# Optimization experiments

Measured on AMD Instinct MI355X. Metric: run time of the kernel, lower is better.

Reference implementation:

```python
import jax, jax.numpy as jnp
import numpy as np

RF = 13          # receptive field with defaults
N_LAYERS = 8     # blocks(4) * layers(2)
DIMS = 32
RC = 16          # residual/dilation channels
SC = 8           # skip channels
BN_EPS = 1e-5


def conv1x1(x, W, b=None):
    # x: (B,Cin,N,T), W: (Cout,Cin)
    y = jnp.einsum('oc,bcnt->bont', W, x)
    if b is not None:
        y = y + b[None, :, None, None]
    return y


def bn_eval(x, g, b):
    # eval-mode BatchNorm2d with running_mean=0, running_var=1
    return x * (g / jnp.sqrt(1.0 + BN_EPS))[None, :, None, None] + b[None, :, None, None]


def setup_inputs() -> dict:
    key = jax.random.key(0)
    ks = jax.random.split(key, 24)
    B, N, T, days = 16, 1024, 12, 288
    inp = {}
    inp['inputs'] = jax.random.normal(ks[0], (B, 2, N, T), dtype=jnp.float32)
    inp['ind'] = jax.random.randint(ks[1], (B,), 0, days)
    # start convs (1 -> RC)
    inp['start_w'] = jax.random.normal(ks[2], (RC, 1)) * 0.05
    inp['start_b'] = jax.random.normal(ks[3], (RC,)) * 0.05
    inp['starta_w'] = jax.random.normal(ks[4], (RC, 1)) * 0.05
    inp['starta_b'] = jax.random.normal(ks[5], (RC,)) * 0.05
    # dynamic-graph node embeddings (torch.randn init)
    inp['p1'] = jax.random.normal(ks[6], (days, DIMS))
    inp['p2'] = jax.random.normal(ks[7], (N, DIMS))
    inp['p3'] = jax.random.normal(ks[8], (N, DIMS))
    inp['pk'] = jax.random.normal(ks[9], (DIMS, DIMS, DIMS))
    # shared channel-attention fcs (bias=False)
    inp['fc1_w'] = jax.random.normal(ks[10], (RC, RC)) * 0.05
    inp['fc2_w'] = jax.random.normal(ks[11], (RC, RC)) * 0.05
    # per-layer skip convs (RC -> SC)
    inp['skip_w'] = jax.random.normal(ks[12], (N_LAYERS, SC, RC)) * 0.05
    inp['skip_b'] = jax.random.normal(ks[13], (N_LAYERS, SC)) * 0.05
    # per-layer gcn mlp ((order*support_len+1)*RC = 48 -> RC)
    inp['gconv_w'] = jax.random.normal(ks[14], (N_LAYERS, RC, 3 * RC)) * 0.05
    inp['gconv_b'] = jax.random.normal(ks[15], (N_LAYERS, RC)) * 0.05
    # batchnorm affine params
    inp['bn_g'] = jnp.ones((N_LAYERS, RC)) + jax.random.normal(ks[16], (N_LAYERS, RC)) * 0.01
    inp['bn_b'] = jax.random.normal(ks[17], (N_LAYERS, RC)) * 0.01
    inp['bna_g'] = jnp.ones((N_LAYERS, RC)) + jax.random.normal(ks[18], (N_LAYERS, RC)) * 0.01
    inp['bna_b'] = jax.random.normal(ks[19], (N_LAYERS, RC)) * 0.01
    # end convs: 832 -> 64 -> 12
    inp['end1_w'] = jax.random.normal(ks[20], (64, SC * RF * N_LAYERS)) * 0.02
    inp['end1_b'] = jax.random.normal(ks[21], (64,)) * 0.02
    inp['end2_w'] = jax.random.normal(ks[22], (12, 64)) * 0.02
    inp['end2_b'] = jax.random.normal(ks[23], (12,)) * 0.02
    return inp


def reference(inputs, ind, start_w, start_b, starta_w, starta_b, p1, p2, p3, pk,
              fc1_w, fc2_w, skip_w, skip_b, gconv_w, gconv_b,
              bn_g, bn_b, bna_g, bna_b, end1_w, end1_b, end2_w, end2_b):
    B, _, N, T = inputs.shape
    if T < RF:  # static python condition
        xo = jnp.pad(inputs, ((0, 0), (0, 0), (0, 0), (RF - T, 0)))
    else:
        xo = inputs
    x = conv1x1(xo[:, 0:1], start_w, start_b)      # (B,RC,N,RF)
    x_a = conv1x1(xo[:, 1:2], starta_w, starta_b)  # (B,RC,N,RF)

    # dgconstruct: dynamic adjacency (identical for every layer -> compute once)
    te = p1[ind]                                   # (B,DIMS)
    adp = jnp.einsum('ai,ijk->ajk', te, pk)        # (B,DIMS,DIMS)
    src = jnp.einsum('bj,ajk->abk', p2, adp)       # (B,N,DIMS)
    full = jnp.einsum('ck,abk->abc', p3, src)      # (B,N,N)
    temp = full[:, :, :DIMS]                       # (B,N,DIMS)
    x1 = jnp.einsum('bnd,bmd->bnm', src, temp)     # (B,N,N)
    A = jax.nn.relu(jnp.tanh(x1 - jnp.swapaxes(x1, 1, 2)))  # x2 = x1^T

    skips = []
    for i in range(N_LAYERS):
        residual = x
        # avg-pool / max-pool to same size are identity -> avg_out == max_out
        a_out = conv1x1(jax.nn.relu(conv1x1(residual, fc1_w)), fc2_w)
        x = jax.nn.sigmoid(a_out + a_out + x)
        residual_a = x_a
        s = conv1x1(x, skip_w[i], skip_b[i])        # (B,SC,N,RF)
        skips.append(jnp.transpose(s, (0, 1, 3, 2)).reshape(B, SC * RF, N, 1))
        # gcn with support_len=1, order=2 (dropout off in eval)
        h1 = jnp.einsum('bcvl,bwv->bcwl', x, A)
        h2 = jnp.einsum('bcvl,bwv->bcwl', h1, A)
        h = jnp.concatenate([x, h1, h2], axis=1)    # (B,3*RC,N,RF)
        x = conv1x1(h, gconv_w[i], gconv_b[i])
        x = x_a + x
        x_a = x_a + residual_a
        x = x + residual
        x = bn_eval(x, bn_g[i], bn_b[i])
        x_a = bn_eval(x_a, bna_g[i], bna_b[i])

    # torch prepends each new skip: last layer's skip goes first
    skip = jnp.concatenate(skips[::-1], axis=1)     # (B,832,N,1)
    out = jax.nn.relu(skip)
    out = jax.nn.relu(conv1x1(out, end1_w, end1_b))
    out = conv1x1(out, end2_w, end2_b)              # (B,12,N,1)
    return out
```

## Files before the change

### kernel.cpp

```cpp
#include <hip/hip_runtime.h>
#include <math.h>

#define NB 16
#define NCH 16
#define NL 13
#define NN 1024
#define NT 12
#define NLAY 8
#define MROWS 208
#define MPAD 256

typedef _Float16 f16;
typedef __attribute__((ext_vector_type(8))) _Float16 f16x8;
typedef __attribute__((ext_vector_type(16))) float f32x16;

#define OFF_TAB   0
#define OFF_SRC   1024
#define OFF_TEMP  (OFF_SRC  + (size_t)NB*NN*32)
#define OFF_AH    (OFF_TEMP + (size_t)NB*NN*32)
#define OFF_XH    (OFF_AH   + (size_t)NB*NN*NN/2)
#define OFF_XL    (OFF_XH   + (size_t)NB*MPAD*NN/2)
#define OFF_H1H   (OFF_XL   + (size_t)NB*MPAD*NN/2)
#define OFF_H1L   (OFF_H1H  + (size_t)NB*MPAD*NN/2)
#define OFF_H2    (OFF_H1L  + (size_t)NB*MPAD*NN/2)
#define OFF_X     (OFF_H2   + (size_t)NB*MPAD*NN)
#define OFF_SKIP  (OFF_X    + (size_t)NB*MROWS*NN)
#define WS_FLOATS (OFF_SKIP + (size_t)NB*832*NN)

__device__ __forceinline__ void gload16(const void* g, void* l) {
    __builtin_amdgcn_global_load_lds(
        (const __attribute__((address_space(1))) unsigned int*)g,
        (__attribute__((address_space(3))) unsigned int*)l,
        16, 0, 0);
}

__device__ __forceinline__ float fast_tanh(float x) {
    float e = __expf(2.0f * x);
    return 1.0f - 2.0f / (e + 1.0f);
}

__global__ void k_tables(const float* __restrict__ bn_g,
                         const float* __restrict__ bna_g, const float* __restrict__ bna_b,
                         const float* __restrict__ sa_w, const float* __restrict__ sa_b,
                         float* __restrict__ tab) {
    int c = threadIdx.x;
    if (c >= 16) return;
    float inv = 1.0f / sqrtf(1.0f + 1e-5f);
    float A = sa_w[c], Bc = sa_b[c];
    for (int i = 0; i < NLAY; i++) {
        tab[i*16 + c]       = bn_g[i*16 + c] * inv;
        tab[128 + i*16 + c] = A;
        tab[256 + i*16 + c] = Bc;
        float ga = bna_g[i*16 + c] * inv;
        A  = 2.0f * ga * A;
        Bc = 2.0f * ga * Bc + bna_b[i*16 + c];
    }
}

__global__ __launch_bounds__(256) void k_startfc(const float* __restrict__ inp,
                        const float* __restrict__ sw, const float* __restrict__ sb,
                        const float* __restrict__ fc1, const float* __restrict__ fc2,
                        const float* __restrict__ skw, const float* __restrict__ skb,
                        float* __restrict__ x, f16* __restrict__ xh, f16* __restrict__ xl,
                        float* __restrict__ skip) {
    __shared__ float W1[256], W2[256], W3[128], B3[8], SW[16], SB[16];
    int t = threadIdx.x;
    if (t < 256) { W1[t] = fc1[t]; W2[t] = fc2[t]; }
    if (t < 128) W3[t] = skw[t];
    if (t < 8)   B3[t] = skb[t];
    if (t < 16)  { SW[t] = sw[t]; SB[t] = sb[t]; }
    __syncthreads();
    int idx = blockIdx.x*256 + t;
    int n = idx & 1023;
    int q = idx >> 10;
    int l = q % 13, b = q / 13;
    float u = (l == 0) ? 0.f : inp[((size_t)(b*2 + 0)*NN + n)*NT + (l - 1)];
    float v[16], t1[16], v2[16];
    #pragma unroll
    for (int c = 0; c < 16; c++) {
        v[c] = SW[c]*u + SB[c];
        x[((size_t)b*MROWS + c*13 + l)*NN + n] = v[c];
    }
    #pragma unroll
    for (int c = 0; c < 16; c++) {
        float s = 0.f;
        #pragma unroll
        for (int j = 0; j < 16; j++) s += W1[c*16 + j] * v[j];
        t1[c] = fmaxf(s, 0.f);
    }
    #pragma unroll
    for (int c = 0; c < 16; c++) {
        float s = 0.f;
        #pragma unroll
        for (int j = 0; j < 16; j++) s += W2[c*16 + j] * t1[j];
        float z = 2.f*s + v[c];
        v2[c] = 1.f / (1.f + __expf(-z));
        size_t o = ((size_t)b*MPAD + c*13 + l)*NN + n;
        f16 hi = (f16)v2[c];
        xh[o] = hi;
        xl[o] = (f16)(v2[c] - (float)hi);
    }
    #pragma unroll
    for (int sc = 0; sc < 8; sc++) {
        float s = B3[sc];
        #pragma unroll
        for (int c = 0; c < 16; c++) s += W3[sc*16 + c] * v2[c];
        skip[((size_t)b*832 + 7*104 + sc*13 + l)*NN + n] = s;
    }
}

__global__ __launch_bounds__(256) void k_srctemp(const float* __restrict__ p1, const int* __restrict__ ind,
                          const float* __restrict__ pk, const float* __restrict__ p2,
                          const float* __restrict__ p3,
                          float* __restrict__ src, float* __restrict__ temp) {
    __shared__ float te[32];
    __shared__ float adp[32][32];
    __shared__ float M[32][32];
    __shared__ float p3s[32][32];
    int b = blockIdx.x, t = threadIdx.x;
    if (t < 32) te[t] = p1[(size_t)ind[b]*32 + t];
    for (int i = t; i < 1024; i += 256) p3s[i >> 5][i & 31] = p3[i];
    __syncthreads();
    for (int i = t; i < 1024; i += 256) {
        int j = i >> 5, k = i & 31;
        float s = 0.f;
        for (int q = 0; q < 32; q++) s += te[q] * pk[q*1024 + j*32 + k];
        adp[j][k] = s;
    }
    __syncthreads();
    for (int i = t; i < 1024; i += 256) {
        int j = i >> 5, c = i & 31;
        float s = 0.f;
        for (int k = 0; k < 32; k++) s += adp[j][k] * p3s[c][k];
        M[j][c] = s;
    }
    __syncthreads();
    for (int n0 = 0; n0 < NN; n0 += 8) {
        int n = n0 + (t >> 5), k = t & 31;
        float rs = 0.f, rt = 0.f;
        for (int j = 0; j < 32; j++) {
            float pv = p2[n*32 + j];
            rs += pv * adp[j][k];
            rt += pv * M[j][k];
        }
        src [((size_t)b*NN + n)*32 + k] = rs;
        temp[((size_t)b*NN + n)*32 + k] = rt;
    }
}

__global__ __launch_bounds__(256) void k_A(const float* __restrict__ src, const float* __restrict__ temp,
                    f16* __restrict__ Amat) {
    int b = blockIdx.z;
    int r = blockIdx.x, ti = 0;
    while (r >= 16 - ti) { r -= 16 - ti; ti++; }
    int tj = ti + r;
    int n0 = ti*64, m0 = tj*64;
    __shared__ float sn[64][33], tm[64][33], sm[64][33], tn[64][33];
    __shared__ f16 At[64][72];
    int t = threadIdx.x;
    const float* sb_ = src  + (size_t)b*NN*32;
    const float* tb_ = temp + (size_t)b*NN*32;
    for (int i = t; i < 64*32; i += 256) {
        int rr = i >> 5, k = i & 31;
        sn[rr][k] = sb_[(n0 + rr)*32 + k];
        tm[rr][k] = tb_[(m0 + rr)*32 + k];
        sm[rr][k] = sb_[(m0 + rr)*32 + k];
        tn[rr][k] = tb_[(n0 + rr)*32 + k];
    }
    __syncthreads();
    int tr = (t >> 4) * 4, tc = (t & 15) * 4;
    float acc1[4][4] = {}, acc2[4][4] = {};
    for (int k = 0; k < 32; k++) {
        float a[4], bb[4], c2[4], d2[4];
        #pragma unroll
        for (int i = 0; i < 4; i++) { a[i]=sn[tr+i][k]; bb[i]=tm[tc+i][k]; c2[i]=sm[tc+i][k]; d2[i]=tn[tr+i][k]; }
        #pragma unroll
        for (int i = 0; i < 4; i++)
            #pragma unroll
            for (int j = 0; j < 4; j++) { acc1[i][j] += a[i]*bb[j]; acc2[i][j] += c2[j]*d2[i]; }
    }
    #pragma unroll
    for (int i = 0; i < 4; i++)
        #pragma unroll
        for (int j = 0; j < 4; j++) {
            float v = fast_tanh(acc1[i][j] - acc2[i][j]);
            Amat[((size_t)b*NN + n0 + tr + i)*NN + m0 + tc + j] = (f16)(v > 0.f ? v : 0.f);
            At[tc + j][tr + i] = (f16)(-v > 0.f ? -v : 0.f);
        }
    __syncthreads();
    for (int i = t; i < 512; i += 256) {
        int rr = i >> 3, c8 = (i & 7) * 8;
        f16* dst = &Amat[((size_t)b*NN + m0 + rr)*NN + n0 + c8];
        #pragma unroll
        for (int k = 0; k < 8; k++) dst[k] = At[rr][c8 + k];
    }
}

template<bool HOP1>
__global__ __launch_bounds__(256) void k_gmm(const f16* __restrict__ Xh, const f16* __restrict__ Xl,
                     const f16* __restrict__ Ag, float* __restrict__ Cf,
                     f16* __restrict__ Ch, f16* __restrict__ Cl) {
    __shared__ alignas(16) f16 As[128*64];
    __shared__ alignas(16) f16 Xs[2*64*64];
    const int bid = blockIdx.x;
    const int xcd = bid & 7;
    const int j   = bid >> 3;
    const int b   = xcd + ((j >> 5) << 3);
    const int tile = j & 31;
    const int my  = tile >> 3;
    const int n0  = (tile & 7) * 128;
    const int t = threadIdx.x;
    const int w = t >> 6, lane = t & 63;
    const char* Ab  = (const char*)(Ag + (size_t)b*NN*NN);
    const char* Xhb = (const char*)(Xh + (size_t)b*MPAD*NN);
    const char* Xlb = (const char*)(Xl + (size_t)b*MPAD*NN);

    const int wm = (w >> 1) * 32, wn = (w & 1) * 64;
    const int kh = lane >> 5;
    const int arow = wm + (lane & 31);
    const int brow0 = wn + (lane & 31);
    const int brow1 = brow0 + 32;
    const char* aP0 = (const char*)Xs + (size_t)arow*128;
    const char* aP1 = aP0 + 8192;
    const char* bP0 = (const char*)As + (size_t)brow0*128;
    const char* bP1 = (const char*)As + (size_t)brow1*128;
    const int swa = arow & 7, swb0 = brow0 & 7, swb1 = brow1 & 7;

    f32x16 acc0 = {}, acc1 = {};

    for (int k0 = 0; k0 < NN; k0 += 64) {
        const char* Abase = Ab + (size_t)n0*2048 + (size_t)k0*2;
        #pragma unroll
        for (int rr = 0; rr < 4; ++rr) {
            int q = rr*4 + w;
            int slot = q*64 + lane;
            int row = slot >> 3, ch = slot & 7;
            gload16(Abase + (size_t)row*2048 + ((ch ^ (row & 7)) << 4),
                    (char*)As + (size_t)q*1024);
        }
        const char* Xb0 = Xhb + (size_t)(my*64)*2048 + (size_t)k0*2;
        const char* Xb1 = Xlb + (size_t)(my*64)*2048 + (size_t)k0*2;
        #pragma unroll
        for (int rr = 0; rr < 4; ++rr) {
            int q = rr*4 + w;
            int slot = q*64 + lane;
            int row = (slot >> 3) & 63, ch = slot & 7;
            const char* base = (q >> 3) ? Xb1 : Xb0;
            gload16(base + (size_t)row*2048 + ((ch ^ (row & 7)) << 4),
                    (char*)Xs + (size_t)q*1024);
        }
        __syncthreads();
        #pragma unroll
        for (int s = 0; s < 4; ++s) {
            int cn = s*2 + kh;
            f16x8 ah = *(const f16x8*)(aP0 + ((cn ^ swa) << 4));
            f16x8 al = *(const f16x8*)(aP1 + ((cn ^ swa) << 4));
            f16x8 b0 = *(const f16x8*)(bP0 + ((cn ^ swb0) << 4));
            f16x8 b1 = *(const f16x8*)(bP1 + ((cn ^ swb1) << 4));
            acc0 = __builtin_amdgcn_mfma_f32_32x32x16_f16(ah, b0, acc0, 0, 0, 0);
            acc1 = __builtin_amdgcn_mfma_f32_32x32x16_f16(ah, b1, acc1, 0, 0, 0);
            acc0 = __builtin_amdgcn_mfma_f32_32x32x16_f16(al, b0, acc0, 0, 0, 0);
            acc1 = __builtin_amdgcn_mfma_f32_32x32x16_f16(al, b1, acc1, 0, 0, 0);
        }
        __syncthreads();
    }

    const int coll = lane & 31;
    #pragma unroll
    for (int reg = 0; reg < 16; ++reg) {
        int m = my*64 + wm + (reg & 3) + 8*(reg >> 2) + 4*kh;
        if (m < MROWS) {
            size_t o0 = ((size_t)b*MPAD + m)*NN + n0 + wn + coll;
            float v0 = acc0[reg], v1 = acc1[reg];
            if (HOP1) {
                f16 h0 = (f16)v0; Ch[o0]      = h0; Cl[o0]      = (f16)(v0 - (float)h0);
                f16 h1 = (f16)v1; Ch[o0 + 32] = h1; Cl[o0 + 32] = (f16)(v1 - (float)h1);
            } else {
                Cf[o0] = v0; Cf[o0 + 32] = v1;
            }
        }
    }
}

__global__ __launch_bounds__(256) void k_epifc(float* __restrict__ x,
                      f16* __restrict__ xh, f16* __restrict__ xl,
                      const f16* __restrict__ h1h, const f16* __restrict__ h1l,
                      const float* __restrict__ h2,
                      const float* __restrict__ inp, const float* __restrict__ gw,
                      const float* __restrict__ gb, const float* __restrict__ bnb,
                      const float* __restrict__ tab,
                      const float* __restrict__ fc1, const float* __restrict__ fc2,
                      const float* __restrict__ skw, const float* __restrict__ skb,
                      float* __restrict__ skip, int layer) {
    __shared__ float W[768], W1[256], W2[256], W3[128], B3[8];
    __shared__ float GB[16], BNBs[16], BNS[16], AC[16], BC[16];
    int t = threadIdx.x;
    for (int i = t; i < 768; i += 256) W[i] = gw[layer*768 + i];
    if (t < 256) { W1[t] = fc1[t]; W2[t] = fc2[t]; }
    int nl = layer + 1;
    if (t < 128) W3[t] = skw[nl*128 + t];
    if (t < 8)   B3[t] = skb[nl*8 + t];
    if (t < 16) {
        GB[t]   = gb[layer*16 + t];
        BNBs[t] = bnb[layer*16 + t];
        BNS[t]  = tab[layer*16 + t];
        AC[t]   = tab[128 + layer*16 + t];
        BC[t]   = tab[256 + layer*16 + t];
    }
    __syncthreads();
    int idx = blockIdx.x*256 + t;
    int n = idx & 1023;
    int q = idx >> 10;
    int l = q % 13, b = q / 13;
    float u1 = (l == 0) ? 0.f : inp[((size_t)(b*2 + 1)*NN + n)*NT + (l - 1)];
    float vx[16], v1[16], v2[16], xnew[16];
    #pragma unroll
    for (int c = 0; c < 16; c++) {
        size_t op = ((size_t)b*MPAD + c*13 + l)*NN + n;
        vx[c] = (float)xh[op] + (float)xl[op];
        v1[c] = (float)h1h[op] + (float)h1l[op];
        v2[c] = h2[op];
    }
    #pragma unroll
    for (int o = 0; o < 16; o++) {
        float s = GB[o];
        #pragma unroll
        for (int c = 0; c < 16; c++) s += W[o*48 + c]      * vx[c];
        #pragma unroll
        for (int c = 0; c < 16; c++) s += W[o*48 + 16 + c] * v1[c];
        #pragma unroll
        for (int c = 0; c < 16; c++) s += W[o*48 + 32 + c] * v2[c];
        float xa = AC[o]*u1 + BC[o];
        float vo = x[((size_t)b*MROWS + o*13 + l)*NN + n];
        xnew[o] = BNS[o]*(s + xa + vo) + BNBs[o];
    }
    if (layer < 6) {
        #pragma unroll
        for (int o = 0; o < 16; o++)
            x[((size_t)b*MROWS + o*13 + l)*NN + n] = xnew[o];
    }
    float t1[16], vs[16];
    #pragma unroll
    for (int c = 0; c < 16; c++) {
        float s = 0.f;
        #pragma unroll
        for (int j = 0; j < 16; j++) s += W1[c*16 + j] * xnew[j];
        t1[c] = fmaxf(s, 0.f);
    }
    #pragma unroll
    for (int c = 0; c < 16; c++) {
        float s = 0.f;
        #pragma unroll
        for (int j = 0; j < 16; j++) s += W2[c*16 + j] * t1[j];
        float z = 2.f*s + xnew[c];
        vs[c] = 1.f / (1.f + __expf(-z));
        if (layer < 6) {
            size_t o = ((size_t)b*MPAD + c*13 + l)*NN + n;
            f16 hi = (f16)vs[c];
            xh[o] = hi;
            xl[o] = (f16)(vs[c] - (float)hi);
        }
    }
    #pragma unroll
    for (int sc = 0; sc < 8; sc++) {
        float s = B3[sc];
        #pragma unroll
        for (int c = 0; c < 16; c++) s += W3[sc*16 + c] * vs[c];
        skip[((size_t)b*832 + (7 - nl)*104 + sc*13 + l)*NN + n] = s;
    }
}

__global__ __launch_bounds__(256) void k_end1(const float* __restrict__ skip, const float* __restrict__ w1,
                       float* __restrict__ out1) {
    __shared__ alignas(16) float Ws[52][68];
    __shared__ alignas(16) float Ss[52][68];
    int n0 = blockIdx.x * 64, ks = blockIdx.y, b = blockIdx.z;
    int t = threadIdx.x, ty = t >> 4, tx = t & 15;
    float acc[4][4] = {};
    int kbase = ks * 208;
    for (int kk = 0; kk < 4; kk++) {
        int k0 = kbase + kk*52;
        for (int i = t; i < 52*64; i += 256) {
            int r = i >> 6, c = i & 63;
            float sv = skip[((size_t)b*832 + k0 + r)*NN + n0 + c];
            Ss[r][c] = sv > 0.f ? sv : 0.f;
            Ws[r][c] = w1[(size_t)c*832 + k0 + r];
        }
        __syncthreads();
        #pragma unroll 4
        for (int k = 0; k < 52; k++) {
            float4 av = *(const float4*)&Ws[k][ty*4];
            float4 bv = *(const float4*)&Ss[k][tx*4];
            float a[4] = {av.x, av.y, av.z, av.w};
            float bb[4] = {bv.x, bv.y, bv.z, bv.w};
            #pragma unroll
            for (int i = 0; i < 4; i++)
                #pragma unroll
                for (int jj = 0; jj < 4; jj++) acc[i][jj] += a[i]*bb[jj];
        }
        __syncthreads();
    }
    #pragma unroll
    for (int i = 0; i < 4; i++)
        #pragma unroll
        for (int jj = 0; jj < 4; jj++)
            out1[(((size_t)ks*NB + b)*64 + ty*4 + i)*NN + n0 + tx*4 + jj] = acc[i][jj];
}

__global__ __launch_bounds__(256) void k_end2(const float* __restrict__ out1, const float* __restrict__ b1,
                       const float* __restrict__ w2, const float* __restrict__ b2,
                       float* __restrict__ outp) {
    __shared__ float S[64][68];
    int n0 = blockIdx.x * 64, b = blockIdx.y;
    int t = threadIdx.x;
    for (int i = t; i < 4096; i += 256) {
        int o = i >> 6, n = i & 63;
        float s = b1[o];
        #pragma unroll
        for (int ks = 0; ks < 4; ks++)
            s += out1[(((size_t)ks*NB + b)*64 + o)*NN + n0 + n];
        S[o][n] = s > 0.f ? s : 0.f;
    }
    __syncthreads();
    for (int idx = t; idx < 12*64; idx += 256) {
        int jr = idx >> 6, n = idx & 63;
        float s = b2[jr];
        for (int o = 0; o < 64; o++) s += w2[jr*64 + o] * S[o][n];
        outp[((size_t)b*12 + jr)*NN + n0 + n] = s;
    }
}

extern "C" void kernel_launch(void* const* d_in, const int* in_sizes, int n_in,
                              void* d_out, int out_size, void* d_ws, size_t ws_size,
                              hipStream_t stream) {
    (void)in_sizes; (void)n_in; (void)out_size;
    if (ws_size < WS_FLOATS * sizeof(float)) return;

    const float* inputs  = (const float*)d_in[0];
    const int*   ind     = (const int*)  d_in[1];
    const float* start_w = (const float*)d_in[2];
    const float* start_b = (const float*)d_in[3];
    const float* starta_w= (const float*)d_in[4];
    const float* starta_b= (const float*)d_in[5];
    const float* p1      = (const float*)d_in[6];
    const float* p2      = (const float*)d_in[7];
    const float* p3      = (const float*)d_in[8];
    const float* pk      = (const float*)d_in[9];
    const float* fc1_w   = (const float*)d_in[10];
    const float* fc2_w   = (const float*)d_in[11];
    const float* skip_w  = (const float*)d_in[12];
    const float* skip_b  = (const float*)d_in[13];
    const float* gconv_w = (const float*)d_in[14];
    const float* gconv_b = (const float*)d_in[15];
    const float* bn_g    = (const float*)d_in[16];
    const float* bn_b    = (const float*)d_in[17];
    const float* bna_g   = (const float*)d_in[18];
    const float* bna_b   = (const float*)d_in[19];
    const float* end1_w  = (const float*)d_in[20];
    const float* end1_b  = (const float*)d_in[21];
    const float* end2_w  = (const float*)d_in[22];
    const float* end2_b  = (const float*)d_in[23];

    float* ws   = (float*)d_ws;
    float* tab  = ws + OFF_TAB;
    float* src  = ws + OFF_SRC;
    float* temp = ws + OFF_TEMP;
    f16*   Ah   = (f16*)(ws + OFF_AH);
    f16*   xh   = (f16*)(ws + OFF_XH);
    f16*   xl   = (f16*)(ws + OFF_XL);
    f16*   h1h  = (f16*)(ws + OFF_H1H);
    f16*   h1l  = (f16*)(ws + OFF_H1L);
    float* h2   = ws + OFF_H2;
    float* x    = ws + OFF_X;
    float* skip = ws + OFF_SKIP;

    k_tables<<<1, 64, 0, stream>>>(bn_g, bna_g, bna_b, starta_w, starta_b, tab);
    k_startfc<<<(NB*NL*NN)/256, 256, 0, stream>>>(inputs, start_w, start_b, fc1_w, fc2_w,
                                                  skip_w, skip_b, x, xh, xl, skip);
    k_srctemp<<<NB, 256, 0, stream>>>(p1, ind, pk, p2, p3, src, temp);
    k_A<<<dim3(136, 1, NB), 256, 0, stream>>>(src, temp, Ah);

    for (int i = 0; i < 7; i++) {
        k_gmm<true ><<<512, 256, 0, stream>>>(xh,  xl,  Ah, nullptr, h1h, h1l);
        k_gmm<false><<<512, 256, 0, stream>>>(h1h, h1l, Ah, h2, nullptr, nullptr);
        k_epifc<<<(NB*NL*NN)/256, 256, 0, stream>>>(x, xh, xl, h1h, h1l, h2, inputs,
                                                    gconv_w, gconv_b, bn_b, tab,
                                                    fc1_w, fc2_w, skip_w, skip_b, skip, i);
    }
    k_end1<<<dim3(16, 4, NB), 256, 0, stream>>>(skip, end1_w, h2);
    k_end2<<<dim3(16, NB), 256, 0, stream>>>(h2, end1_b, end2_w, end2_b, (float*)d_out);
}
```

Measured before the change: 707.9 us.

## Double-buffer GEMM staging, split src/temp kernel, transpose k_A shared tiles

The graph GEMM kernel now double-buffers its A and X tiles in LDS. It issues the next k-slice's global-to-LDS loads before computing the current one, syncing with vmcnt waits and raw barriers. Separately, the single-block-per-batch src/temp computation is split into a small adp/M kernel plus a wider kernel over node chunks that caches p2 in shared memory, giving more parallelism. k_A stores its operands transposed so float4 LDS reads replace scalar ones. The trade-off is twice the LDS per GEMM block, which can lower occupancy, plus one extra kernel launch.

Result: faster. 651.0 us (-8.0%).

```diff
diff --git a/kernel.cpp b/kernel.cpp
--- a/kernel.cpp
+++ b/kernel.cpp
@@ -15,7 +15,9 @@
 typedef __attribute__((ext_vector_type(16))) float f32x16;
 
 #define OFF_TAB   0
-#define OFF_SRC   1024
+#define OFF_ADP   1024
+#define OFF_M     (OFF_ADP  + (size_t)NB*1024)
+#define OFF_SRC   (OFF_M    + (size_t)NB*1024)
 #define OFF_TEMP  (OFF_SRC  + (size_t)NB*NN*32)
 #define OFF_AH    (OFF_TEMP + (size_t)NB*NN*32)
 #define OFF_XH    (OFF_AH   + (size_t)NB*NN*NN/2)
@@ -109,42 +111,53 @@
     }
 }
 
-__global__ __launch_bounds__(256) void k_srctemp(const float* __restrict__ p1, const int* __restrict__ ind,
-                          const float* __restrict__ pk, const float* __restrict__ p2,
-                          const float* __restrict__ p3,
-                          float* __restrict__ src, float* __restrict__ temp) {
+__global__ __launch_bounds__(256) void k_adp(const float* __restrict__ p1, const int* __restrict__ ind,
+                      const float* __restrict__ pk, const float* __restrict__ p3,
+                      float* __restrict__ adpg, float* __restrict__ Mg) {
     __shared__ float te[32];
     __shared__ float adp[32][32];
-    __shared__ float M[32][32];
     __shared__ float p3s[32][32];
     int b = blockIdx.x, t = threadIdx.x;
     if (t < 32) te[t] = p1[(size_t)ind[b]*32 + t];
     for (int i = t; i < 1024; i += 256) p3s[i >> 5][i & 31] = p3[i];
     __syncthreads();
     for (int i = t; i < 1024; i += 256) {
-        int j = i >> 5, k = i & 31;
         float s = 0.f;
-        for (int q = 0; q < 32; q++) s += te[q] * pk[q*1024 + j*32 + k];
-        adp[j][k] = s;
+        for (int q = 0; q < 32; q++) s += te[q] * pk[q*1024 + i];
+        adp[i >> 5][i & 31] = s;
+        adpg[(size_t)b*1024 + i] = s;
     }
     __syncthreads();
     for (int i = t; i < 1024; i += 256) {
         int j = i >> 5, c = i & 31;
         float s = 0.f;
         for (int k = 0; k < 32; k++) s += adp[j][k] * p3s[c][k];
-        M[j][c] = s;
-    }
-    __syncthreads();
-    for (int n0 = 0; n0 < NN; n0 += 8) {
-        int n = n0 + (t >> 5), k = t & 31;
+        Mg[(size_t)b*1024 + i] = s;
+    }
+}
+
+__global__ __launch_bounds__(256) void k_st(const float* __restrict__ p2, const float* __restrict__ adpg,
+                     const float* __restrict__ Mg,
+                     float* __restrict__ src, float* __restrict__ temp) {
+    __shared__ float adpS[32][32], MS[32][32], p2S[128][32];
+    int b = blockIdx.y, n0 = blockIdx.x * 128, t = threadIdx.x;
+    for (int i = t; i < 1024; i += 256) {
+        adpS[i >> 5][i & 31] = adpg[(size_t)b*1024 + i];
+        MS[i >> 5][i & 31]   = Mg[(size_t)b*1024 + i];
+    }
+    for (int i = t; i < 128*32; i += 256) p2S[i >> 5][i & 31] = p2[(size_t)(n0 + (i >> 5))*32 + (i & 31)];
+    __syncthreads();
+    int k = t & 31, g = t >> 5;
+    for (int nn = g; nn < 128; nn += 8) {
         float rs = 0.f, rt = 0.f;
+        #pragma unroll 8
         for (int j = 0; j < 32; j++) {
-            float pv = p2[n*32 + j];
-            rs += pv * adp[j][k];
-            rt += pv * M[j][k];
-        }
-        src [((size_t)b*NN + n)*32 + k] = rs;
-        temp[((size_t)b*NN + n)*32 + k] = rt;
+            float pv = p2S[nn][j];
+            rs += pv * adpS[j][k];
+            rt += pv * MS[j][k];
+        }
+        src [((size_t)b*NN + n0 + nn)*32 + k] = rs;
+        temp[((size_t)b*NN + n0 + nn)*32 + k] = rt;
     }
 }
 
@@ -155,37 +168,43 @@
     while (r >= 16 - ti) { r -= 16 - ti; ti++; }
     int tj = ti + r;
     int n0 = ti*64, m0 = tj*64;
-    __shared__ float sn[64][33], tm[64][33], sm[64][33], tn[64][33];
+    __shared__ float snT[32][68], tmT[32][68], smT[32][68], tnT[32][68];
     __shared__ f16 At[64][72];
     int t = threadIdx.x;
     const float* sb_ = src  + (size_t)b*NN*32;
     const float* tb_ = temp + (size_t)b*NN*32;
     for (int i = t; i < 64*32; i += 256) {
         int rr = i >> 5, k = i & 31;
-        sn[rr][k] = sb_[(n0 + rr)*32 + k];
-        tm[rr][k] = tb_[(m0 + rr)*32 + k];
-        sm[rr][k] = sb_[(m0 + rr)*32 + k];
-        tn[rr][k] = tb_[(n0 + rr)*32 + k];
+        snT[k][rr] = sb_[(n0 + rr)*32 + k];
+        tmT[k][rr] = tb_[(m0 + rr)*32 + k];
+        smT[k][rr] = sb_[(m0 + rr)*32 + k];
+        tnT[k][rr] = tb_[(n0 + rr)*32 + k];
     }
     __syncthreads();
     int tr = (t >> 4) * 4, tc = (t & 15) * 4;
     float acc1[4][4] = {}, acc2[4][4] = {};
+    #pragma unroll 4
     for (int k = 0; k < 32; k++) {
-        float a[4], bb[4], c2[4], d2[4];
-        #pragma unroll
-        for (int i = 0; i < 4; i++) { a[i]=sn[tr+i][k]; bb[i]=tm[tc+i][k]; c2[i]=sm[tc+i][k]; d2[i]=tn[tr+i][k]; }
+        float4 a  = *(const float4*)&snT[k][tr];
+        float4 bb = *(const float4*)&tmT[k][tc];
+        float4 c2 = *(const float4*)&smT[k][tc];
+        float4 d2 = *(const float4*)&tnT[k][tr];
+        float av[4] = {a.x, a.y, a.z, a.w};
+        float bv[4] = {bb.x, bb.y, bb.z, bb.w};
+        float cv[4] = {c2.x, c2.y, c2.z, c2.w};
+        float dv[4] = {d2.x, d2.y, d2.z, d2.w};
         #pragma unroll
         for (int i = 0; i < 4; i++)
             #pragma unroll
-            for (int j = 0; j < 4; j++) { acc1[i][j] += a[i]*bb[j]; acc2[i][j] += c2[j]*d2[i]; }
+            for (int jj = 0; jj < 4; jj++) { acc1[i][jj] += av[i]*bv[jj]; acc2[i][jj] += cv[jj]*dv[i]; }
     }
     #pragma unroll
     for (int i = 0; i < 4; i++)
         #pragma unroll
-        for (int j = 0; j < 4; j++) {
-            float v = fast_tanh(acc1[i][j] - acc2[i][j]);
-            Amat[((size_t)b*NN + n0 + tr + i)*NN + m0 + tc + j] = (f16)(v > 0.f ? v : 0.f);
-            At[tc + j][tr + i] = (f16)(-v > 0.f ? -v : 0.f);
+        for (int jj = 0; jj < 4; jj++) {
+            float v = fast_tanh(acc1[i][jj] - acc2[i][jj]);
+            Amat[((size_t)b*NN + n0 + tr + i)*NN + m0 + tc + jj] = (f16)(v > 0.f ? v : 0.f);
+            At[tc + jj][tr + i] = (f16)(-v > 0.f ? -v : 0.f);
         }
     __syncthreads();
     for (int i = t; i < 512; i += 256) {
@@ -200,8 +219,8 @@
 __global__ __launch_bounds__(256) void k_gmm(const f16* __restrict__ Xh, const f16* __restrict__ Xl,
                      const f16* __restrict__ Ag, float* __restrict__ Cf,
                      f16* __restrict__ Ch, f16* __restrict__ Cl) {
-    __shared__ alignas(16) f16 As[128*64];
-    __shared__ alignas(16) f16 Xs[2*64*64];
+    __shared__ alignas(16) f16 As[2][128*64];
+    __shared__ alignas(16) f16 Xs[2][2*64*64];
     const int bid = blockIdx.x;
     const int xcd = bid & 7;
     const int j   = bid >> 3;
@@ -215,41 +234,50 @@
     const char* Xhb = (const char*)(Xh + (size_t)b*MPAD*NN);
     const char* Xlb = (const char*)(Xl + (size_t)b*MPAD*NN);
 
+    const char* asrc[4];
+    int adst[4];
+    const char* xsrc[4];
+    int xdst[4];
+    {
+        const char* Abase = Ab + (size_t)n0*2048;
+        const char* Xb0 = Xhb + (size_t)(my*64)*2048;
+        const char* Xb1 = Xlb + (size_t)(my*64)*2048;
+        #pragma unroll
+        for (int rr = 0; rr < 4; ++rr) {
+            int q = rr*4 + w;
+            int slot = q*64 + lane;
+            int row = slot >> 3, ch = slot & 7;
+            asrc[rr] = Abase + (size_t)row*2048 + ((ch ^ (row & 7)) << 4);
+            adst[rr] = q*1024;
+            int xrow = row & 63;
+            xsrc[rr] = ((q >> 3) ? Xb1 : Xb0) + (size_t)xrow*2048 + ((ch ^ (xrow & 7)) << 4);
+            xdst[rr] = q*1024;
+        }
+    }
+
     const int wm = (w >> 1) * 32, wn = (w & 1) * 64;
     const int kh = lane >> 5;
     const int arow = wm + (lane & 31);
     const int brow0 = wn + (lane & 31);
     const int brow1 = brow0 + 32;
-    const char* aP0 = (const char*)Xs + (size_t)arow*128;
-    const char* aP1 = aP0 + 8192;
-    const char* bP0 = (const char*)As + (size_t)brow0*128;
-    const char* bP1 = (const char*)As + (size_t)brow1*128;
     const int swa = arow & 7, swb0 = brow0 & 7, swb1 = brow1 & 7;
 
     f32x16 acc0 = {}, acc1 = {};
 
-    for (int k0 = 0; k0 < NN; k0 += 64) {
-        const char* Abase = Ab + (size_t)n0*2048 + (size_t)k0*2;
-        #pragma unroll
-        for (int rr = 0; rr < 4; ++rr) {
-            int q = rr*4 + w;
-            int slot = q*64 + lane;
-            int row = slot >> 3, ch = slot & 7;
-            gload16(Abase + (size_t)row*2048 + ((ch ^ (row & 7)) << 4),
-                    (char*)As + (size_t)q*1024);
-        }
-        const char* Xb0 = Xhb + (size_t)(my*64)*2048 + (size_t)k0*2;
-        const char* Xb1 = Xlb + (size_t)(my*64)*2048 + (size_t)k0*2;
-        #pragma unroll
-        for (int rr = 0; rr < 4; ++rr) {
-            int q = rr*4 + w;
-            int slot = q*64 + lane;
-            int row = (slot >> 3) & 63, ch = slot & 7;
-            const char* base = (q >> 3) ? Xb1 : Xb0;
-            gload16(base + (size_t)row*2048 + ((ch ^ (row & 7)) << 4),
-                    (char*)Xs + (size_t)q*1024);
-        }
-        __syncthreads();
+    auto stage = [&](int buf, int it) {
+        size_t koff = (size_t)it * 128;
+        #pragma unroll
+        for (int rr = 0; rr < 4; ++rr)
+            gload16(asrc[rr] + koff, (char*)As[buf] + adst[rr]);
+        #pragma unroll
+        for (int rr = 0; rr < 4; ++rr)
+            gload16(xsrc[rr] + koff, (char*)Xs[buf] + xdst[rr]);
+    };
+    auto compute = [&](int buf) {
+        const char* aP0 = (const char*)Xs[buf] + (size_t)arow*128;
+        const char* aP1 = aP0 + 8192;
+        const char* bP0 = (const char*)As[buf] + (size_t)brow0*128;
+        const char* bP1 = (const char*)As[buf] + (size_t)brow1*128;
         #pragma unroll
         for (int s = 0; s < 4; ++s) {
             int cn = s*2 + kh;
@@ -262,8 +290,21 @@
             acc0 = __builtin_amdgcn_mfma_f32_32x32x16_f16(al, b0, acc0, 0, 0, 0);
             acc1 = __builtin_amdgcn_mfma_f32_32x32x16_f16(al, b1, acc1, 0, 0, 0);
         }
-        __syncthreads();
-    }
+    };
+
+    stage(0, 0);
+    int cur = 0;
+    for (int it = 0; it < 15; ++it) {
+        stage(cur ^ 1, it + 1);
+        asm volatile("s_waitcnt vmcnt(8)" ::: "memory");
+        __builtin_amdgcn_s_barrier();
+        compute(cur);
+        __builtin_amdgcn_s_barrier();
+        cur ^= 1;
+    }
+    asm volatile("s_waitcnt vmcnt(0)" ::: "memory");
+    __builtin_amdgcn_s_barrier();
+    compute(cur);
 
     const int coll = lane & 31;
     #pragma unroll
@@ -463,6 +504,8 @@
 
     float* ws   = (float*)d_ws;
     float* tab  = ws + OFF_TAB;
+    float* adpg = ws + OFF_ADP;
+    float* Mg   = ws + OFF_M;
     float* src  = ws + OFF_SRC;
     float* temp = ws + OFF_TEMP;
     f16*   Ah   = (f16*)(ws + OFF_AH);
@@ -477,7 +520,8 @@
     k_tables<<<1, 64, 0, stream>>>(bn_g, bna_g, bna_b, starta_w, starta_b, tab);
     k_startfc<<<(NB*NL*NN)/256, 256, 0, stream>>>(inputs, start_w, start_b, fc1_w, fc2_w,
                                                   skip_w, skip_b, x, xh, xl, skip);
-    k_srctemp<<<NB, 256, 0, stream>>>(p1, ind, pk, p2, p3, src, temp);
+    k_adp<<<NB, 256, 0, stream>>>(p1, ind, pk, p3, adpg, Mg);
+    k_st<<<dim3(8, NB), 256, 0, stream>>>(p2, adpg, Mg, src, temp);
     k_A<<<dim3(136, 1, NB), 256, 0, stream>>>(src, temp, Ah);
 
     for (int i = 0; i < 7; i++) {
```
